# Kernel optimization log

Hardware: AMD Instinct MI355X
Metric: run time of the kernel (lower is better)

The kernel has to match this reference:

```python
import jax, jax.numpy as jnp
import numpy as np

D_MODEL = 1024
N_HIDDEN = 64   # per-head dim (outer factor of packed proj dim)
N_HEAD = 16
B, L = 2, 2048


def setup_inputs() -> dict:
    key = jax.random.key(0)
    ks = jax.random.split(key, 7)
    s = 0.02
    return {
        "q": jax.random.normal(ks[0], (B, L, D_MODEL), dtype=jnp.float32),
        "k": jax.random.normal(ks[1], (B, L, D_MODEL), dtype=jnp.float32),
        "v": jax.random.normal(ks[2], (B, L, D_MODEL), dtype=jnp.float32),
        # torch nn.Linear weights: shape (out_features, in_features), y = x @ W.T
        "W_Q": jax.random.normal(ks[3], (N_HIDDEN * N_HEAD, D_MODEL), dtype=jnp.float32) * s,
        "W_K": jax.random.normal(ks[4], (N_HIDDEN * N_HEAD, D_MODEL), dtype=jnp.float32) * s,
        "W_V": jax.random.normal(ks[5], (N_HIDDEN * N_HEAD, D_MODEL), dtype=jnp.float32) * s,
        "W_O": jax.random.normal(ks[6], (D_MODEL, N_HEAD * N_HIDDEN), dtype=jnp.float32) * s,
    }


def reference(q, k, v, W_Q, W_K, W_V, W_O):
    b, l, _ = q.shape
    # projections (bias=False)
    qp = q @ W_Q.T  # [b,l,n_hidden*n_head]
    kp = k @ W_K.T
    vp = v @ W_V.T
    # rearrange 'b l (c h) -> b l c h' with c=n_hidden: hidden is OUTER factor
    qh = qp.reshape(b, l, N_HIDDEN, N_HEAD)
    kh = kp.reshape(b, l, N_HIDDEN, N_HEAD)
    vh = vp.reshape(b, l, N_HIDDEN, N_HEAD)
    scores = jnp.einsum('bldh,bjdh->bhlj', qh, kh) / np.float32(np.sqrt(N_HIDDEN))
    attn = jax.nn.softmax(scores, axis=-1)
    out = jnp.einsum('bhlj,bjdh->bldh', attn, vh)  # [b,l,n_hidden,n_head]
    out = out.reshape(b, l, N_HIDDEN * N_HEAD)      # 'b l d h -> b l (d h)'
    return out @ W_O.T
```

## Files before the change

kernel.cpp:

```cpp
#include <hip/hip_runtime.h>
#include <hip/hip_bf16.h>
#include <stdint.h>

typedef __attribute__((ext_vector_type(8))) short short8;
typedef __attribute__((ext_vector_type(4))) float f32x4;
typedef __attribute__((ext_vector_type(16))) float f32x16;
typedef __attribute__((ext_vector_type(2))) int int2v;
typedef unsigned short u16;
typedef unsigned int u32;


#define WAIT_VM8() do { asm volatile("s_waitcnt vmcnt(8)" ::: "memory"); \
                        __builtin_amdgcn_sched_barrier(0); } while (0)
#define WAIT_VM0() do { asm volatile("s_waitcnt vmcnt(0)" ::: "memory"); \
                        __builtin_amdgcn_sched_barrier(0); } while (0)
#define BARRIER()  do { __builtin_amdgcn_s_barrier(); \
                        __builtin_amdgcn_sched_barrier(0); } while (0)

__device__ __forceinline__ u16 bf16rne(float f) {
  u32 u = __builtin_bit_cast(u32, f);
  u += 0x7FFFu + ((u >> 16) & 1u);
  return (u16)(u >> 16);
}

__device__ __forceinline__ u32 cvtpk(float lo, float hi) {
  u32 r;
  asm("v_cvt_pk_bf16_f32 %0, %1, %2" : "=v"(r) : "v"(lo), "v"(hi));
  return r;
}

__device__ __forceinline__ void gl_lds16(const u16* g, u16* l) {
  __builtin_amdgcn_global_load_lds((const __attribute__((address_space(1))) void*)g,
                                   (__attribute__((address_space(3))) void*)l, 16, 0, 0);
}

struct CastArgs {
  const float* src[7];
  u16* dst[7];
  int n4[7];
};

__global__ void cast_all(CastArgs a) {
  const int id = blockIdx.y;
  const float* __restrict__ s = a.src[id];
  u16* __restrict__ d = a.dst[id];
  const int stride = gridDim.x * blockDim.x;
  const int i0 = blockIdx.x * blockDim.x + threadIdx.x;
  if (id < 6) {
    const int n4 = a.n4[id];
    for (int i = i0; i < n4; i += stride) {
      float4 v = ((const float4*)s)[i];
      u32 lo = (u32)bf16rne(v.x) | ((u32)bf16rne(v.y) << 16);
      u32 hi = (u32)bf16rne(v.z) | ((u32)bf16rne(v.w) << 16);
      ((uint2*)d)[i] = make_uint2(lo, hi);
    }
  } else {
    const int n = a.n4[6];
    for (int i = i0; i < n; i += stride) {
      int row = i >> 10, c = i & 1023;
      int hh = c >> 6, dd = c & 63;
      d[i] = bf16rne(s[(row << 10) + dd * 16 + hh]);
    }
  }
}

template<int AHEADS>
__device__ __forceinline__ void gemm_body(const u16* __restrict__ A, const u16* __restrict__ Bw,
                                          void* __restrict__ Cd, int epi, float ascale) {
  const int bn = blockIdx.x * 128, bm = blockIdx.y * 128;
  const int tid = threadIdx.x, lane = tid & 63, w = tid >> 6;
  const int wr = w >> 1, wc = w & 1;
  __shared__ __align__(16) u16 As[2][128 * 64];
  __shared__ __align__(16) u16 Bs[2][128 * 64];
  f32x4 acc[4][4];
#pragma unroll
  for (int m = 0; m < 4; ++m)
#pragma unroll
    for (int n = 0; n < 4; ++n) acc[m][n] = (f32x4){0.f, 0.f, 0.f, 0.f};

  auto STAGE = [&](int kt, int b) {
#pragma unroll
    for (int i = 0; i < 4; ++i) {
      int c = tid + i * 256;
      int row = c >> 3, kc = c & 7;
      int swz = (kc ^ (row & 7)) << 3;
      const u16* srcA;
      if (AHEADS) {
        int bA = bm >> 11;
        int lrow = (bm & 2047) + row;
        srcA = A + ((size_t)(bA * 16 + kt) * 2048 + lrow) * 64 + swz;
      } else {
        srcA = A + (size_t)(bm + row) * 1024 + kt * 64 + swz;
      }
      gl_lds16(srcA, &As[b][c * 8]);
      const u16* srcB = Bw + (size_t)(bn + row) * 1024 + kt * 64 + swz;
      gl_lds16(srcB, &Bs[b][c * 8]);
    }
  };

  auto COMPUTE = [&](int b) {
#pragma unroll
    for (int ks = 0; ks < 2; ++ks) {
      const int ck = ks * 4 + (lane >> 4);
      short8 af[4], bfr[4];
#pragma unroll
      for (int m = 0; m < 4; ++m) {
        int r = wr * 64 + m * 16 + (lane & 15);
        af[m] = *(const short8*)&As[b][(r * 8 + (ck ^ (r & 7))) * 8];
      }
#pragma unroll
      for (int n = 0; n < 4; ++n) {
        int r = wc * 64 + n * 16 + (lane & 15);
        bfr[n] = *(const short8*)&Bs[b][(r * 8 + (ck ^ (r & 7))) * 8];
      }
#pragma unroll
      for (int m = 0; m < 4; ++m)
#pragma unroll
        for (int n = 0; n < 4; ++n)
          acc[m][n] = __builtin_amdgcn_mfma_f32_16x16x32_bf16(af[m], bfr[n], acc[m][n], 0, 0, 0);
    }
  };

  STAGE(0, 0);
  STAGE(1, 1);
  for (int kt = 0; kt < 15; ++kt) {
    WAIT_VM8();
    BARRIER();
    COMPUTE(kt & 1);
    BARRIER();
    if (kt < 14) STAGE(kt + 2, kt & 1);
  }
  WAIT_VM0();
  BARRIER();
  COMPUTE(1);

  const int lrow4 = (lane >> 4) << 2;
  const int h = lane & 15;
  if (epi == 0) {
    u16* D = (u16*)Cd;
    const int dbase = (bn + wc * 64) >> 4;
#pragma unroll
    for (int m = 0; m < 4; ++m)
#pragma unroll
      for (int i = 0; i < 4; ++i) {
        int R = bm + wr * 64 + m * 16 + lrow4 + i;
        int b = R >> 11, l = R & 2047;
        u32 lo = (u32)bf16rne(acc[m][0][i] * ascale) | ((u32)bf16rne(acc[m][1][i] * ascale) << 16);
        u32 hi = (u32)bf16rne(acc[m][2][i] * ascale) | ((u32)bf16rne(acc[m][3][i] * ascale) << 16);
        size_t addr = ((size_t)((b * 16 + h) * 2048 + l)) * 64 + dbase;
        *(uint2*)(D + addr) = make_uint2(lo, hi);
      }
  } else if (epi == 1) {
    u16* D = (u16*)Cd;
    const int dbase = (bn + wc * 64) >> 4;
    const int b = bm >> 11;
#pragma unroll
    for (int m = 0; m < 4; ++m) {
      int l0 = (bm & 2047) + wr * 64 + m * 16 + lrow4;
#pragma unroll
      for (int n = 0; n < 4; ++n) {
        int d = dbase + n;
        u32 lo = (u32)bf16rne(acc[m][n][0]) | ((u32)bf16rne(acc[m][n][1]) << 16);
        u32 hi = (u32)bf16rne(acc[m][n][2]) | ((u32)bf16rne(acc[m][n][3]) << 16);
        size_t addr = ((size_t)((b * 16 + h) * 64 + d)) * 2048 + l0;
        *(uint2*)(D + addr) = make_uint2(lo, hi);
      }
    }
  } else {
    float* D = (float*)Cd;
#pragma unroll
    for (int m = 0; m < 4; ++m)
#pragma unroll
      for (int i = 0; i < 4; ++i) {
        int R = bm + wr * 64 + m * 16 + lrow4 + i;
        size_t base = (size_t)R * 1024 + bn + wc * 64 + (lane & 15);
#pragma unroll
        for (int n = 0; n < 4; ++n) D[base + n * 16] = acc[m][n][i];
      }
  }
}

struct ProjArgs { const u16* A[3]; const u16* W[3]; u16* D[3]; float scale[3]; };

__global__ __launch_bounds__(256, 2) void gemm_proj(ProjArgs pa) {
  const int z = blockIdx.z;
  gemm_body<0>(pa.A[z], pa.W[z], pa.D[z], z == 2 ? 1 : 0, pa.scale[z]);
}

__global__ __launch_bounds__(256, 2) void gemm_oproj(const u16* __restrict__ A,
                                                     const u16* __restrict__ W,
                                                     float* __restrict__ C) {
  gemm_body<1>(A, W, C, 2, 1.0f);
}

__global__ __launch_bounds__(128, 2) void attn_kernel(const u16* __restrict__ Qh,
                                                      const u16* __restrict__ Kh,
                                                      const u16* __restrict__ Vt,
                                                      u16* __restrict__ Oh) {
  const int hb = blockIdx.x;
  const int qt = blockIdx.y;
  const int tid = threadIdx.x, lane = tid & 63, w = tid >> 6;
  const int l31 = lane & 31, hi = lane >> 5;
  __shared__ __align__(16) u16 Ks[2][64 * 64];
  __shared__ __align__(16) u16 Vs[2][64 * 64];

  const u16* Qg = Qh + (size_t)hb * (2048 * 64);
  const u16* Kg = Kh + (size_t)hb * (2048 * 64);
  const u16* Vg = Vt + (size_t)hb * (64 * 2048);
  const int qrow = qt * 64 + w * 32 + l31;

  short8 qf[4];
#pragma unroll
  for (int ks = 0; ks < 4; ++ks)
    qf[ks] = *(const short8*)(Qg + (size_t)qrow * 64 + ks * 16 + hi * 8);

  int rs[4], sw[4];
#pragma unroll
  for (int i = 0; i < 4; ++i) {
    int c = tid + i * 128;
    rs[i] = c >> 3;
    sw[i] = (((c & 7) ^ (rs[i] & 7)) << 3);
  }

  auto STAGE = [&](int t, int b) {
    const size_t ko = (size_t)t * (64 * 64);
    const int vo = t * 64;
#pragma unroll
    for (int i = 0; i < 4; ++i) {
      int c = tid + i * 128;
      gl_lds16(Kg + ko + (size_t)rs[i] * 64 + sw[i], &Ks[b][c * 8]);
      gl_lds16(Vg + (size_t)rs[i] * 2048 + vo + sw[i], &Vs[b][c * 8]);
    }
  };

  f32x16 oacc0 = {}, oacc1 = {};
  float lrow = 0.f;

  auto COMPUTE = [&](int b) {
    f32x16 s0 = {}, s1 = {};
    __builtin_amdgcn_s_setprio(1);
#pragma unroll
    for (int ks = 0; ks < 4; ++ks) {
      const int ck = 2 * ks + hi;
      const int r0 = l31, r1 = 32 + l31;
      short8 k0 = *(const short8*)&Ks[b][(r0 * 8 + (ck ^ (r0 & 7))) * 8];
      short8 k1 = *(const short8*)&Ks[b][(r1 * 8 + (ck ^ (r1 & 7))) * 8];
      s0 = __builtin_amdgcn_mfma_f32_32x32x16_bf16(k0, qf[ks], s0, 0, 0, 0);
      s1 = __builtin_amdgcn_mfma_f32_32x32x16_bf16(k1, qf[ks], s1, 0, 0, 0);
    }
    __builtin_amdgcn_s_setprio(0);

#pragma unroll
    for (int i = 0; i < 16; ++i) {
      s0[i] = __builtin_amdgcn_exp2f(s0[i]);
      s1[i] = __builtin_amdgcn_exp2f(s1[i]);
    }
    {
      f32x16 a01 = s0 + s1;
      float r8[8];
#pragma unroll
      for (int i = 0; i < 8; ++i) r8[i] = a01[i] + a01[i + 8];
#pragma unroll
      for (int i = 0; i < 4; ++i) r8[i] += r8[i + 4];
      float rsum = (r8[0] + r8[1]) + (r8[2] + r8[3]);
      int2v pr = __builtin_amdgcn_permlane32_swap(__builtin_bit_cast(int, rsum),
                                                  __builtin_bit_cast(int, rsum), false, false);
      lrow += __builtin_bit_cast(float, pr[0]) + __builtin_bit_cast(float, pr[1]);
    }

#pragma unroll
    for (int c = 0; c < 4; ++c) {
      float pe0, pe1, pe2, pe3, pe4, pe5, pe6, pe7;
      if (c < 2) {
        const int s8 = (c & 1) * 8;
        pe0 = s0[s8 + 0]; pe1 = s0[s8 + 1]; pe2 = s0[s8 + 2]; pe3 = s0[s8 + 3];
        pe4 = s0[s8 + 4]; pe5 = s0[s8 + 5]; pe6 = s0[s8 + 6]; pe7 = s0[s8 + 7];
      } else {
        const int s8 = (c & 1) * 8;
        pe0 = s1[s8 + 0]; pe1 = s1[s8 + 1]; pe2 = s1[s8 + 2]; pe3 = s1[s8 + 3];
        pe4 = s1[s8 + 4]; pe5 = s1[s8 + 5]; pe6 = s1[s8 + 6]; pe7 = s1[s8 + 7];
      }
      u32 a0 = cvtpk(pe0, pe1), a1 = cvtpk(pe2, pe3);
      u32 a2 = cvtpk(pe4, pe5), a3 = cvtpk(pe6, pe7);
      int2v w02 = __builtin_amdgcn_permlane32_swap((int)a0, (int)a2, false, false);
      int2v w13 = __builtin_amdgcn_permlane32_swap((int)a1, (int)a3, false, false);
      union { u32 wu[4]; short8 v; } un;
      un.wu[0] = (u32)w02[0]; un.wu[1] = (u32)w13[0];
      un.wu[2] = (u32)w02[1]; un.wu[3] = (u32)w13[1];
      const int ckv = 2 * c + hi;
      const int rv0 = l31, rv1 = 32 + l31;
      short8 v0 = *(const short8*)&Vs[b][(rv0 * 8 + (ckv ^ (rv0 & 7))) * 8];
      short8 v1 = *(const short8*)&Vs[b][(rv1 * 8 + (ckv ^ (rv1 & 7))) * 8];
      __builtin_amdgcn_s_setprio(1);
      oacc0 = __builtin_amdgcn_mfma_f32_32x32x16_bf16(v0, un.v, oacc0, 0, 0, 0);
      oacc1 = __builtin_amdgcn_mfma_f32_32x32x16_bf16(v1, un.v, oacc1, 0, 0, 0);
      __builtin_amdgcn_s_setprio(0);
    }
  };

  STAGE(0, 0);
  STAGE(1, 1);
  for (int t = 0; t < 31; ++t) {
    WAIT_VM8();
    BARRIER();
    COMPUTE(t & 1);
    BARRIER();
    if (t < 30) STAGE(t + 2, t & 1);
  }
  WAIT_VM0();
  BARRIER();
  COMPUTE(1);

  const float inv = 1.0f / lrow;
  u16* Og = Oh + (size_t)hb * (2048 * 64) + (size_t)qrow * 64;
#pragma unroll
  for (int dblk = 0; dblk < 2; ++dblk) {
#pragma unroll
    for (int r = 0; r < 16; r += 2) {
      const int d = dblk * 32 + (r & 3) + 8 * (r >> 2) + 4 * hi;
      float v0 = (dblk ? oacc1[r] : oacc0[r]) * inv;
      float v1 = (dblk ? oacc1[r + 1] : oacc0[r + 1]) * inv;
      *(u32*)(Og + d) = (u32)bf16rne(v0) | ((u32)bf16rne(v1) << 16);
    }
  }
}

extern "C" void kernel_launch(void* const* d_in, const int* in_sizes, int n_in,
                              void* d_out, int out_size, void* d_ws, size_t ws_size,
                              hipStream_t stream) {
  const float* q = (const float*)d_in[0];
  const float* k = (const float*)d_in[1];
  const float* v = (const float*)d_in[2];
  const float* WQ = (const float*)d_in[3];
  const float* WK = (const float*)d_in[4];
  const float* WV = (const float*)d_in[5];
  const float* WO = (const float*)d_in[6];
  float* out = (float*)d_out;
  char* ws = (char*)d_ws;
  const size_t MB = 1024 * 1024;
  if (ws_size < 64 * MB) return;

  u16* qb  = (u16*)(ws + 0 * MB);
  u16* kb  = (u16*)(ws + 8 * MB);
  u16* vb  = (u16*)(ws + 16 * MB);
  u16* WQb = (u16*)(ws + 24 * MB);
  u16* WKb = (u16*)(ws + 26 * MB);
  u16* WVb = (u16*)(ws + 28 * MB);
  u16* WOt = (u16*)(ws + 30 * MB);
  u16* Qh  = (u16*)(ws + 32 * MB);
  u16* Kh  = (u16*)(ws + 40 * MB);
  u16* Vt  = (u16*)(ws + 48 * MB);
  u16* Ohd = (u16*)(ws + 56 * MB);

  CastArgs ca;
  ca.src[0] = q;  ca.dst[0] = qb;  ca.n4[0] = (4096 * 1024) / 4;
  ca.src[1] = k;  ca.dst[1] = kb;  ca.n4[1] = (4096 * 1024) / 4;
  ca.src[2] = v;  ca.dst[2] = vb;  ca.n4[2] = (4096 * 1024) / 4;
  ca.src[3] = WQ; ca.dst[3] = WQb; ca.n4[3] = (1024 * 1024) / 4;
  ca.src[4] = WK; ca.dst[4] = WKb; ca.n4[4] = (1024 * 1024) / 4;
  ca.src[5] = WV; ca.dst[5] = WVb; ca.n4[5] = (1024 * 1024) / 4;
  ca.src[6] = WO; ca.dst[6] = WOt; ca.n4[6] = 1024 * 1024;
  cast_all<<<dim3(256, 7), 256, 0, stream>>>(ca);

  ProjArgs pa;
  pa.A[0] = qb; pa.W[0] = WQb; pa.D[0] = Qh;  pa.scale[0] = 0.18033688011f;
  pa.A[1] = kb; pa.W[1] = WKb; pa.D[1] = Kh;  pa.scale[1] = 1.0f;
  pa.A[2] = vb; pa.W[2] = WVb; pa.D[2] = Vt;  pa.scale[2] = 1.0f;
  gemm_proj<<<dim3(8, 32, 3), 256, 0, stream>>>(pa);

  attn_kernel<<<dim3(32, 32), 128, 0, stream>>>(Qh, Kh, Vt, Ohd);

  gemm_oproj<<<dim3(8, 32), 256, 0, stream>>>(Ohd, WOt, out);
}
```

Measured before the change: 138.4 us.

## Software-pipeline attention loop: overlap QK^T, softmax and PV across key tiles

Splits the per-tile attention compute into separate QK^T, softmax and PV stages and runs them skewed across iterations. Each step computes QK^T for tile t, PV for tile t-2 and softmax for tile t-1. K and V loads are staged separately, with a third V buffer in LDS because V is consumed two tiles later. The aim is to hide exp and permute latency behind MFMA work. The cost is more live registers for two score sets and packed probabilities, which could hurt occupancy or cause spills, plus extra LDS.

```diff
diff --git a/kernel.cpp b/kernel.cpp
--- a/kernel.cpp
+++ b/kernel.cpp
@@ -202,7 +202,7 @@
   const int tid = threadIdx.x, lane = tid & 63, w = tid >> 6;
   const int l31 = lane & 31, hi = lane >> 5;
   __shared__ __align__(16) u16 Ks[2][64 * 64];
-  __shared__ __align__(16) u16 Vs[2][64 * 64];
+  __shared__ __align__(16) u16 Vs[3][64 * 64];
 
   const u16* Qg = Qh + (size_t)hb * (2048 * 64);
   const u16* Kg = Kh + (size_t)hb * (2048 * 64);
@@ -222,52 +222,78 @@
     sw[i] = (((c & 7) ^ (rs[i] & 7)) << 3);
   }
 
-  auto STAGE = [&](int t, int b) {
+  auto STAGE_K = [&](int t, int slot) {
     const size_t ko = (size_t)t * (64 * 64);
-    const int vo = t * 64;
 #pragma unroll
     for (int i = 0; i < 4; ++i) {
       int c = tid + i * 128;
-      gl_lds16(Kg + ko + (size_t)rs[i] * 64 + sw[i], &Ks[b][c * 8]);
-      gl_lds16(Vg + (size_t)rs[i] * 2048 + vo + sw[i], &Vs[b][c * 8]);
-    }
-  };
-
-  f32x16 oacc0 = {}, oacc1 = {};
+      gl_lds16(Kg + ko + (size_t)rs[i] * 64 + sw[i], &Ks[slot][c * 8]);
+    }
+  };
+  auto STAGE_V = [&](int t, int slot) {
+    const int vo = t * 64;
+#pragma unroll
+    for (int i = 0; i < 4; ++i) {
+      int c = tid + i * 128;
+      gl_lds16(Vg + (size_t)rs[i] * 2048 + vo + sw[i], &Vs[slot][c * 8]);
+    }
+  };
+
+  f32x16 oacc0, oacc1, SA0, SA1, SB0, SB1;
+#pragma unroll
+  for (int i = 0; i < 16; ++i) { oacc0[i] = 0.f; oacc1[i] = 0.f; }
+  u32 pkA[16], pkB[16];
   float lrow = 0.f;
 
-  auto COMPUTE = [&](int b) {
-    f32x16 s0 = {}, s1 = {};
+  auto QKT = [&](int kslot, f32x16& s0, f32x16& s1) {
+#pragma unroll
+    for (int i = 0; i < 16; ++i) { s0[i] = 0.f; s1[i] = 0.f; }
     __builtin_amdgcn_s_setprio(1);
 #pragma unroll
     for (int ks = 0; ks < 4; ++ks) {
       const int ck = 2 * ks + hi;
       const int r0 = l31, r1 = 32 + l31;
-      short8 k0 = *(const short8*)&Ks[b][(r0 * 8 + (ck ^ (r0 & 7))) * 8];
-      short8 k1 = *(const short8*)&Ks[b][(r1 * 8 + (ck ^ (r1 & 7))) * 8];
+      short8 k0 = *(const short8*)&Ks[kslot][(r0 * 8 + (ck ^ (r0 & 7))) * 8];
+      short8 k1 = *(const short8*)&Ks[kslot][(r1 * 8 + (ck ^ (r1 & 7))) * 8];
       s0 = __builtin_amdgcn_mfma_f32_32x32x16_bf16(k0, qf[ks], s0, 0, 0, 0);
       s1 = __builtin_amdgcn_mfma_f32_32x32x16_bf16(k1, qf[ks], s1, 0, 0, 0);
     }
     __builtin_amdgcn_s_setprio(0);
-
+  };
+
+  auto PV = [&](const u32* pk, int vslot) {
+    __builtin_amdgcn_s_setprio(1);
+#pragma unroll
+    for (int c = 0; c < 4; ++c) {
+      union { u32 wu[4]; short8 v; } un;
+      un.wu[0] = pk[c * 4 + 0]; un.wu[1] = pk[c * 4 + 1];
+      un.wu[2] = pk[c * 4 + 2]; un.wu[3] = pk[c * 4 + 3];
+      const int ckv = 2 * c + hi;
+      const int rv0 = l31, rv1 = 32 + l31;
+      short8 v0 = *(const short8*)&Vs[vslot][(rv0 * 8 + (ckv ^ (rv0 & 7))) * 8];
+      short8 v1 = *(const short8*)&Vs[vslot][(rv1 * 8 + (ckv ^ (rv1 & 7))) * 8];
+      oacc0 = __builtin_amdgcn_mfma_f32_32x32x16_bf16(v0, un.v, oacc0, 0, 0, 0);
+      oacc1 = __builtin_amdgcn_mfma_f32_32x32x16_bf16(v1, un.v, oacc1, 0, 0, 0);
+    }
+    __builtin_amdgcn_s_setprio(0);
+  };
+
+  auto SOFTMAX = [&](f32x16& s0, f32x16& s1, u32* pk) {
 #pragma unroll
     for (int i = 0; i < 16; ++i) {
       s0[i] = __builtin_amdgcn_exp2f(s0[i]);
       s1[i] = __builtin_amdgcn_exp2f(s1[i]);
     }
-    {
-      f32x16 a01 = s0 + s1;
-      float r8[8];
-#pragma unroll
-      for (int i = 0; i < 8; ++i) r8[i] = a01[i] + a01[i + 8];
-#pragma unroll
-      for (int i = 0; i < 4; ++i) r8[i] += r8[i + 4];
-      float rsum = (r8[0] + r8[1]) + (r8[2] + r8[3]);
-      int2v pr = __builtin_amdgcn_permlane32_swap(__builtin_bit_cast(int, rsum),
-                                                  __builtin_bit_cast(int, rsum), false, false);
-      lrow += __builtin_bit_cast(float, pr[0]) + __builtin_bit_cast(float, pr[1]);
-    }
-
+    f32x16 a01 = s0 + s1;
+    float r8[8];
+#pragma unroll
+    for (int i = 0; i < 8; ++i) r8[i] = a01[i] + a01[i + 8];
+#pragma unroll
+    for (int i = 0; i < 4; ++i) r8[i] += r8[i + 4];
+    float rsum = (r8[0] + r8[1]) + (r8[2] + r8[3]);
+    int2v pr = __builtin_amdgcn_permlane32_swap(__builtin_bit_cast(int, rsum),
+                                                __builtin_bit_cast(int, rsum), false, false);
+    lrow += __builtin_bit_cast(float, pr[0]) + __builtin_bit_cast(float, pr[1]);
 #pragma unroll
     for (int c = 0; c < 4; ++c) {
       float pe0, pe1, pe2, pe3, pe4, pe5, pe6, pe7;
@@ -284,32 +310,43 @@
       u32 a2 = cvtpk(pe4, pe5), a3 = cvtpk(pe6, pe7);
       int2v w02 = __builtin_amdgcn_permlane32_swap((int)a0, (int)a2, false, false);
       int2v w13 = __builtin_amdgcn_permlane32_swap((int)a1, (int)a3, false, false);
-      union { u32 wu[4]; short8 v; } un;
-      un.wu[0] = (u32)w02[0]; un.wu[1] = (u32)w13[0];
-      un.wu[2] = (u32)w02[1]; un.wu[3] = (u32)w13[1];
-      const int ckv = 2 * c + hi;
-      const int rv0 = l31, rv1 = 32 + l31;
-      short8 v0 = *(const short8*)&Vs[b][(rv0 * 8 + (ckv ^ (rv0 & 7))) * 8];
-      short8 v1 = *(const short8*)&Vs[b][(rv1 * 8 + (ckv ^ (rv1 & 7))) * 8];
-      __builtin_amdgcn_s_setprio(1);
-      oacc0 = __builtin_amdgcn_mfma_f32_32x32x16_bf16(v0, un.v, oacc0, 0, 0, 0);
-      oacc1 = __builtin_amdgcn_mfma_f32_32x32x16_bf16(v1, un.v, oacc1, 0, 0, 0);
-      __builtin_amdgcn_s_setprio(0);
-    }
-  };
-
-  STAGE(0, 0);
-  STAGE(1, 1);
-  for (int t = 0; t < 31; ++t) {
-    WAIT_VM8();
+      pk[c * 4 + 0] = (u32)w02[0]; pk[c * 4 + 1] = (u32)w13[0];
+      pk[c * 4 + 2] = (u32)w02[1]; pk[c * 4 + 3] = (u32)w13[1];
+    }
+  };
+
+  STAGE_K(0, 0); STAGE_K(1, 1); STAGE_V(0, 0);
+  WAIT_VM8(); BARRIER();
+  QKT(0, SA0, SA1);
+  BARRIER();
+  STAGE_K(2, 0); STAGE_V(1, 1);
+  WAIT_VM8(); BARRIER();
+  QKT(1, SB0, SB1);
+  SOFTMAX(SA0, SA1, pkB);
+  BARRIER();
+  STAGE_K(3, 1); STAGE_V(2, 2);
+
+  for (int i = 2; i < 32; i += 2) {
+    WAIT_VM8(); BARRIER();
+    QKT(0, SA0, SA1);
+    PV(pkB, (i - 2) % 3);
+    SOFTMAX(SB0, SB1, pkA);
     BARRIER();
-    COMPUTE(t & 1);
+    if (i + 2 <= 31) STAGE_K(i + 2, 0);
+    STAGE_V(i + 1, (i + 1) % 3);
+    WAIT_VM8(); BARRIER();
+    QKT(1, SB0, SB1);
+    PV(pkA, (i - 1) % 3);
+    SOFTMAX(SA0, SA1, pkB);
     BARRIER();
-    if (t < 30) STAGE(t + 2, t & 1);
-  }
-  WAIT_VM0();
-  BARRIER();
-  COMPUTE(1);
+    if (i + 3 <= 31) STAGE_K(i + 3, 1);
+    if (i + 2 <= 31) STAGE_V(i + 2, (i + 2) % 3);
+  }
+
+  WAIT_VM0(); BARRIER();
+  SOFTMAX(SB0, SB1, pkA);
+  PV(pkB, 30 % 3);
+  PV(pkA, 31 % 3);
 
   const float inv = 1.0f / lrow;
   u16* Og = Oh + (size_t)hb * (2048 * 64) + (size_t)qrow * 64;
```

Result: faster. 135.3 us (-2.3%).
